# Performance work log

Hardware: AMD Instinct MI355X
Metric: run time of the kernel (lower is better)

Reference implementation:

```python
import jax, jax.numpy as jnp
import numpy as np

N_NODES = 50000
N_EDGES = 800000
N_GRAPHS = 64
IN_DIM = 128
HID = 128
S, C = 4, 16
DIM1 = 3 * S * S  # 48
OUT_DIM = DIM1 * C  # 768


def gcn_conv(x, W, b, src, dst, w):
    """PyG GCNConv: linear transform, then sym-normalized aggregation with self-loops (weight 1)."""
    n = x.shape[0]
    h = x @ W  # [N, out]
    deg = jnp.zeros((n,), x.dtype).at[dst].add(w) + 1.0  # self-loop weight 1
    dinv = jax.lax.rsqrt(deg)
    norm = dinv[src] * w * dinv[dst]  # [E]
    agg = jnp.zeros_like(h).at[dst].add(h[src] * norm[:, None])
    agg = agg + h * (1.0 / deg)[:, None]  # self-loop messages
    return agg + b


def setup_inputs() -> dict:
    key = jax.random.key(0)
    ks = jax.random.split(key, 16)
    x = jax.random.normal(ks[0], (N_NODES, IN_DIM), jnp.float32)
    edge_index = jax.random.randint(ks[1], (2, N_EDGES), 0, N_NODES, jnp.int64)
    edge_attr = jax.random.uniform(ks[2], (N_EDGES,), jnp.float32)
    batch = jnp.sort(jax.random.randint(ks[3], (N_NODES,), 0, N_GRAPHS, jnp.int64))

    def glorot(k, fan_in, fan_out):
        s = np.sqrt(6.0 / (fan_in + fan_out)).astype(np.float32)
        return jax.random.uniform(k, (fan_in, fan_out), jnp.float32, -s, s)

    return {
        "x": x, "edge_index": edge_index, "edge_attr": edge_attr, "batch": batch,
        "W1": glorot(ks[4], IN_DIM, HID), "b1": jnp.zeros((HID,), jnp.float32),
        "W2": glorot(ks[5], HID, HID // 2), "b2": jnp.zeros((HID // 2,), jnp.float32),
        "W3": glorot(ks[6], HID // 2, HID // 4), "b3": jnp.zeros((HID // 4,), jnp.float32),
        "Wl": glorot(ks[7], HID // 4, OUT_DIM), "bl": jnp.zeros((OUT_DIM,), jnp.float32),
    }


def reference(x, edge_index, edge_attr, batch, W1, b1, W2, b2, W3, b3, Wl, bl):
    src, dst = edge_index[0], edge_index[1]
    w = edge_attr / edge_attr.max()
    h = jax.nn.relu(gcn_conv(x, W1, b1, src, dst, w))
    h = jax.nn.relu(gcn_conv(h, W2, b2, src, dst, w))
    h = jax.nn.relu(gcn_conv(h, W3, b3, src, dst, w))
    # global mean pool over graphs
    sums = jax.ops.segment_sum(h, batch, num_segments=N_GRAPHS)
    cnt = jax.ops.segment_sum(jnp.ones((h.shape[0],), h.dtype), batch, num_segments=N_GRAPHS)
    pooled = sums / jnp.maximum(cnt, 1.0)[:, None]
    out = pooled @ Wl + bl  # [G, OUT_DIM]
    return out.reshape(N_GRAPHS, DIM1, C)
```

## Files before the change

### kernel.cpp

```cpp
#include <hip/hip_runtime.h>
#include <hip/hip_bf16.h>

#define NN 50000
#define NE 800000
#define NG 64
#define OUTD 768

#define G1B ((NN + 63) / 64)
#define SSEG 64
#define TTL 4
#define ESEG (NE / SSEG)
#define NTL (NN / TTL)
#define HRB (SSEG * TTL)
#define WB 16
#define MAXB 128
#define NB 196

#define W1E 2048
#define W2E 1024
#define W3E 256

__device__ __forceinline__ float bflo(unsigned int u) { return __uint_as_float(u << 16); }
__device__ __forceinline__ float bfhi(unsigned int u) { return __uint_as_float(u & 0xffff0000u); }
__device__ __forceinline__ unsigned short f2bf(float f) {
    unsigned int u = __float_as_uint(f);
    return (unsigned short)((u + 0x7fffu + ((u >> 16) & 1u)) >> 16);
}
__device__ __forceinline__ unsigned int pack2bf(float lo, float hi) {
    return (unsigned int)f2bf(lo) | ((unsigned int)f2bf(hi) << 16);
}

typedef __attribute__((ext_vector_type(8))) short bf16x8;
typedef __attribute__((ext_vector_type(4))) float f32x4;
union FragU { uint4 u4; bf16x8 v; };

__global__ __launch_bounds__(256) void prep_kernel(const float* __restrict__ W1,
                                                   const float* __restrict__ W2,
                                                   const float* __restrict__ W3,
                                                   uint4* __restrict__ f1,
                                                   uint4* __restrict__ f2,
                                                   uint4* __restrict__ f3,
                                                   const float* __restrict__ ea,
                                                   unsigned int* wmax) {
    const int b = blockIdx.x;
    if (b < WB) {
        for (int q = b * 256 + threadIdx.x; q < W1E + W2E + W3E; q += WB * 256) {
            const float* W; uint4* F; int N, qq;
            if (q < W1E) { W = W1; F = f1; N = 128; qq = q; }
            else if (q < W1E + W2E) { W = W2; F = f2; N = 64; qq = q - W1E; }
            else { W = W3; F = f3; N = 32; qq = q - W1E - W2E; }
            int lane = qq & 63, fi = qq >> 6;
            int NCT = N / 16, ct = fi % NCT, kc = fi / NCT;
            int col = ct * 16 + (lane & 15);
            int kb = kc * 32 + ((lane >> 4) << 3);
            uint4 w;
            w.x = pack2bf(W[(size_t)(kb + 0) * N + col], W[(size_t)(kb + 1) * N + col]);
            w.y = pack2bf(W[(size_t)(kb + 2) * N + col], W[(size_t)(kb + 3) * N + col]);
            w.z = pack2bf(W[(size_t)(kb + 4) * N + col], W[(size_t)(kb + 5) * N + col]);
            w.w = pack2bf(W[(size_t)(kb + 6) * N + col], W[(size_t)(kb + 7) * N + col]);
            F[qq] = w;
        }
    } else {
        __shared__ float red[256];
        const int bb = b - WB;
        float m = 0.0f;
        for (int i = bb * 256 + threadIdx.x; i < NE; i += MAXB * 256)
            m = fmaxf(m, ea[i]);
        red[threadIdx.x] = m;
        __syncthreads();
        for (int off = 128; off > 0; off >>= 1) {
            if (threadIdx.x < off)
                red[threadIdx.x] = fmaxf(red[threadIdx.x], red[threadIdx.x + off]);
            __syncthreads();
        }
        if (threadIdx.x == 0) atomicMax(wmax, __float_as_uint(red[0]));
    }
}

template <int K, int N, bool SCALE, typename TX>
__device__ __forceinline__ void mfma_gemm_tbl(const TX* __restrict__ X,
                                              const uint4* __restrict__ ftab,
                                              unsigned short* __restrict__ Y,
                                              const float* __restrict__ dinv,
                                              int nRows, int bx) {
    constexpr int NCT = N / 16;
    constexpr int KS = K / 32;
    const int tid = threadIdx.x;
    const int lane = tid & 63;
    const int wv = tid >> 6;
    const int m = lane & 15;
    const int quad = lane >> 4;
    const int row = bx * 64 + wv * 16 + m;
    const bool rowok = row < nRows;
    const TX* xr = X + (size_t)(rowok ? row : 0) * K;

    f32x4 acc[NCT];
#pragma unroll
    for (int ct = 0; ct < NCT; ++ct) acc[ct] = (f32x4){0.f, 0.f, 0.f, 0.f};

#pragma unroll
    for (int kc = 0; kc < KS; ++kc) {
        const int k0 = kc * 32 + quad * 8;
        FragU a;
        if constexpr (sizeof(TX) == 4) {
            float4 a0 = make_float4(0.f, 0.f, 0.f, 0.f), a1 = a0;
            if (rowok) {
                a0 = *(const float4*)(xr + k0);
                a1 = *(const float4*)(xr + k0 + 4);
            }
            a.u4 = make_uint4(pack2bf(a0.x, a0.y), pack2bf(a0.z, a0.w),
                              pack2bf(a1.x, a1.y), pack2bf(a1.z, a1.w));
        } else {
            a.u4 = rowok ? *(const uint4*)(xr + k0) : make_uint4(0, 0, 0, 0);
        }
#pragma unroll
        for (int ct = 0; ct < NCT; ++ct) {
            FragU b;
            b.u4 = ftab[(kc * NCT + ct) * 64 + lane];
            acc[ct] = __builtin_amdgcn_mfma_f32_16x16x32_bf16(a.v, b.v, acc[ct], 0, 0, 0);
        }
    }

    const int orowb = bx * 64 + wv * 16 + quad * 4;
    float dsc[4];
#pragma unroll
    for (int r = 0; r < 4; ++r)
        dsc[r] = SCALE ? ((orowb + r < nRows) ? dinv[orowb + r] : 1.0f) : 1.0f;
#pragma unroll
    for (int ct = 0; ct < NCT; ++ct) {
        int col = ct * 16 + m;
#pragma unroll
        for (int r = 0; r < 4; ++r) {
            int orow = orowb + r;
            if (orow < nRows) Y[(size_t)orow * N + col] = f2bf(dsc[r] * acc[ct][r]);
        }
    }
}

template <int K, int N, bool SCALE, typename TX>
__global__ __launch_bounds__(256) void mfma_gemm_kernel(const TX* __restrict__ X,
                                                        const uint4* __restrict__ ftab,
                                                        unsigned short* __restrict__ Y,
                                                        const float* __restrict__ dinv,
                                                        int nRows) {
    mfma_gemm_tbl<K, N, SCALE>(X, ftab, Y, dinv, nRows, blockIdx.x);
}

__global__ __launch_bounds__(256) void fused1_kernel(const float* __restrict__ x,
                                                     const uint4* __restrict__ f1,
                                                     unsigned short* __restrict__ bufA,
                                                     const int* __restrict__ dst,
                                                     int* __restrict__ rank,
                                                     unsigned short* __restrict__ pcnt) {
    extern __shared__ unsigned int lcnt[];
    const int b = blockIdx.x;
    if (b < G1B) {
        mfma_gemm_tbl<128, 128, false>(x, f1, bufA, nullptr, NN, b);
    } else {
        const int b2 = b - G1B;
        const int seg = b2 >> 2;
        const int tile = b2 & 3;
        for (int i = threadIdx.x; i < NTL / 2; i += 256) lcnt[i] = 0;
        __syncthreads();
        const int base = seg * ESEG;
        const int nlo = tile * NTL;
        for (int e = base + threadIdx.x; e < base + ESEG; e += 256) {
            int d = dst[e] - nlo;
            if ((unsigned)d < (unsigned)NTL) {
                unsigned int add = (d & 1) ? 0x10000u : 1u;
                unsigned int old = atomicAdd(&lcnt[d >> 1], add);
                rank[e] = (int)((old >> ((d & 1) * 16)) & 0xffffu);
            }
        }
        __syncthreads();
        unsigned int* prow32 = (unsigned int*)(pcnt + (size_t)seg * NN + nlo);
        for (int i = threadIdx.x; i < NTL / 2; i += 256) prow32[i] = lcnt[i];
    }
}

__device__ __forceinline__ void gridbar(unsigned int* bar, unsigned int target) {
    __syncthreads();
    if (threadIdx.x == 0) {
        __hip_atomic_fetch_add(bar, 1u, __ATOMIC_ACQ_REL, __HIP_MEMORY_SCOPE_AGENT);
        while (__hip_atomic_load(bar, __ATOMIC_ACQUIRE, __HIP_MEMORY_SCOPE_AGENT) < target)
            __builtin_amdgcn_s_sleep(2);
    }
    __syncthreads();
}

__global__ __launch_bounds__(256) void comb_scan_kernel(unsigned short* __restrict__ pcnt,
                                                        int* __restrict__ rowptr,
                                                        int* __restrict__ blocksum,
                                                        unsigned int* bar) {
    __shared__ int sh[256];
    const int tid = threadIdx.x;
    const int b = blockIdx.x;
    const int n = b * 256 + tid;

    int run = 0;
    if (n < NN) {
#pragma unroll
        for (int s = 0; s < SSEG; ++s) {
            size_t idx = (size_t)s * NN + n;
            int v = pcnt[idx];
            pcnt[idx] = (unsigned short)run;
            run += v;
        }
    }
    sh[tid] = run;
    __syncthreads();
    for (int off = 128; off > 0; off >>= 1) {
        if (tid < off) sh[tid] += sh[tid + off];
        __syncthreads();
    }
    if (tid == 0) blocksum[b] = sh[0];
    gridbar(bar, NB);

    int v2 = (tid < NB) ? blocksum[tid] : 0;
    __syncthreads();
    sh[tid] = v2;
    __syncthreads();
    for (int off = 1; off < 256; off <<= 1) {
        int t = (tid >= off) ? sh[tid - off] : 0;
        __syncthreads();
        sh[tid] += t;
        __syncthreads();
    }
    const int blockoff = (b > 0) ? sh[b - 1] : 0;
    if (b == 0 && tid == 0) rowptr[NN] = sh[NB - 1];
    __syncthreads();
    sh[tid] = run;
    __syncthreads();
    for (int off = 1; off < 256; off <<= 1) {
        int t = (tid >= off) ? sh[tid - off] : 0;
        __syncthreads();
        sh[tid] += t;
        __syncthreads();
    }
    if (n < NN) rowptr[n] = blockoff + sh[tid] - run;
}

__global__ void scat_kernel(const int* __restrict__ src, const int* __restrict__ dst,
                            const float* __restrict__ ea,
                            const int* __restrict__ rowptr,
                            const unsigned short* __restrict__ pcnt,
                            const int* __restrict__ rank,
                            const unsigned int* __restrict__ wmax,
                            int2* __restrict__ epack, int nE) {
    int e = blockIdx.x * blockDim.x + threadIdx.x;
    if (e >= nE) return;
    float rw = 1.0f / __uint_as_float(*wmax);
    int s = e / ESEG;
    int d = dst[e];
    int pos = rowptr[d] + (int)pcnt[(size_t)s * NN + d] + rank[e];
    epack[pos] = make_int2(src[e], __float_as_int(ea[e] * rw));
}

__global__ __launch_bounds__(256) void deg_scale_kernel(const int2* __restrict__ epack,
                                                        const int* __restrict__ rowptr,
                                                        float* __restrict__ dinv,
                                                        unsigned short* __restrict__ bufA) {
    __shared__ float sdinv[256];
    const int tid = threadIdx.x;
    const int b = blockIdx.x;
    const int n = b * 256 + tid;
    float di = 1.0f;
    if (n < NN) {
        int s0 = rowptr[n], s1 = rowptr[n + 1];
        float s = 1.0f;
        for (int e = s0; e < s1; ++e) s += __int_as_float(epack[e].y);
        di = rsqrtf(s);
        dinv[n] = di;
    }
    sdinv[tid] = di;
    __syncthreads();
    const int nrows = min(256, NN - b * 256);
    uint4* rows = (uint4*)bufA + (size_t)b * 256 * 16;
    for (int q = tid; q < nrows * 16; q += 256) {
        const float d = sdinv[q >> 4];
        uint4 u = rows[q];
        u.x = pack2bf(d * bflo(u.x), d * bfhi(u.x));
        u.y = pack2bf(d * bflo(u.y), d * bfhi(u.y));
        u.z = pack2bf(d * bflo(u.z), d * bfhi(u.z));
        u.w = pack2bf(d * bflo(u.w), d * bfhi(u.w));
        rows[q] = u;
    }
}

template <int D>
__global__ __launch_bounds__(256) void agg_kernel(const unsigned short* __restrict__ H,
                                                  const int* __restrict__ rowptr,
                                                  const int2* __restrict__ epack,
                                                  const float* __restrict__ dinv,
                                                  const float* __restrict__ bias,
                                                  unsigned short* __restrict__ out,
                                                  int nNodes) {
    constexpr int LPE = D / 8;
    constexpr int EPW = 64 / LPE;
    const int lane = threadIdx.x & 63;
    const int n = (blockIdx.x << 2) | (threadIdx.x >> 6);
    if (n >= nNodes) return;
    const int esub = lane / LPE;
    const int f8 = (lane % LPE) * 8;
    const int s0 = rowptr[n];
    const int cnt = rowptr[n + 1] - s0;

    float a[8] = {};
    int kb = 0;
    for (; kb + 2 * EPW <= cnt; kb += 2 * EPW) {
        const int2 pa = epack[s0 + kb + esub];
        const int2 pb = epack[s0 + kb + EPW + esub];
        const uint4 ua = *(const uint4*)(H + (size_t)pa.x * D + f8);
        const uint4 ub = *(const uint4*)(H + (size_t)pb.x * D + f8);
        const float ca = __int_as_float(pa.y);
        const float cb = __int_as_float(pb.y);
        a[0] = fmaf(ca, bflo(ua.x), a[0]); a[1] = fmaf(ca, bfhi(ua.x), a[1]);
        a[2] = fmaf(ca, bflo(ua.y), a[2]); a[3] = fmaf(ca, bfhi(ua.y), a[3]);
        a[4] = fmaf(ca, bflo(ua.z), a[4]); a[5] = fmaf(ca, bfhi(ua.z), a[5]);
        a[6] = fmaf(ca, bflo(ua.w), a[6]); a[7] = fmaf(ca, bfhi(ua.w), a[7]);
        a[0] = fmaf(cb, bflo(ub.x), a[0]); a[1] = fmaf(cb, bfhi(ub.x), a[1]);
        a[2] = fmaf(cb, bflo(ub.y), a[2]); a[3] = fmaf(cb, bfhi(ub.y), a[3]);
        a[4] = fmaf(cb, bflo(ub.z), a[4]); a[5] = fmaf(cb, bfhi(ub.z), a[5]);
        a[6] = fmaf(cb, bflo(ub.w), a[6]); a[7] = fmaf(cb, bfhi(ub.w), a[7]);
    }
    for (; kb < cnt; kb += EPW) {
        const int idx = kb + esub;
        const bool ok = idx < cnt;
        const int2 p = ok ? epack[s0 + idx] : make_int2(n, 0);
        const uint4 u = *(const uint4*)(H + (size_t)p.x * D + f8);
        const float c = ok ? __int_as_float(p.y) : 0.f;
        a[0] = fmaf(c, bflo(u.x), a[0]); a[1] = fmaf(c, bfhi(u.x), a[1]);
        a[2] = fmaf(c, bflo(u.y), a[2]); a[3] = fmaf(c, bfhi(u.y), a[3]);
        a[4] = fmaf(c, bflo(u.z), a[4]); a[5] = fmaf(c, bfhi(u.z), a[5]);
        a[6] = fmaf(c, bflo(u.w), a[6]); a[7] = fmaf(c, bfhi(u.w), a[7]);
    }
#pragma unroll
    for (int off = LPE; off < 64; off <<= 1) {
#pragma unroll
        for (int j = 0; j < 8; ++j) a[j] += __shfl_xor(a[j], off);
    }
    if (esub == 0) {
        const float di = dinv[n];
        const uint4 un = *(const uint4*)(H + (size_t)n * D + f8);
        const float4 b0 = *(const float4*)(bias + f8);
        const float4 b1 = *(const float4*)(bias + f8 + 4);
        float o[8];
        o[0] = fmaxf(fmaf(di, a[0] + bflo(un.x), b0.x), 0.f);
        o[1] = fmaxf(fmaf(di, a[1] + bfhi(un.x), b0.y), 0.f);
        o[2] = fmaxf(fmaf(di, a[2] + bflo(un.y), b0.z), 0.f);
        o[3] = fmaxf(fmaf(di, a[3] + bfhi(un.y), b0.w), 0.f);
        o[4] = fmaxf(fmaf(di, a[4] + bflo(un.z), b1.x), 0.f);
        o[5] = fmaxf(fmaf(di, a[5] + bfhi(un.z), b1.y), 0.f);
        o[6] = fmaxf(fmaf(di, a[6] + bflo(un.w), b1.z), 0.f);
        o[7] = fmaxf(fmaf(di, a[7] + bfhi(un.w), b1.w), 0.f);
        uint4 w;
        w.x = pack2bf(o[0], o[1]);
        w.y = pack2bf(o[2], o[3]);
        w.z = pack2bf(o[4], o[5]);
        w.w = pack2bf(o[6], o[7]);
        *(uint4*)(out + (size_t)n * D + f8) = w;
    }
}

__global__ __launch_bounds__(256) void pool2_kernel(const unsigned short* __restrict__ h,
                                                    const int* __restrict__ batch,
                                                    float* __restrict__ pooled, int n) {
    const int g = blockIdx.x;
    int lo = 0, hi = n;
    while (lo < hi) { int m = (lo + hi) >> 1; if (batch[m] < g) lo = m + 1; else hi = m; }
    const int start = lo;
    lo = start; hi = n;
    while (lo < hi) { int m = (lo + hi) >> 1; if (batch[m] < g + 1) lo = m + 1; else hi = m; }
    const int end = lo;

    __shared__ float part[256];
    const int f = threadIdx.x & 31;
    const int r = threadIdx.x >> 5;
    float acc = 0.f;
    for (int i = start + r; i < end; i += 8)
        acc += __uint_as_float((unsigned int)h[(size_t)i * 32 + f] << 16);
    part[threadIdx.x] = acc;
    __syncthreads();
    if (threadIdx.x < 32) {
        float s = 0.f;
#pragma unroll
        for (int q = 0; q < 8; ++q) s += part[q * 32 + f];
        float inv = 1.0f / fmaxf((float)(end - start), 1.0f);
        pooled[g * 32 + f] = s * inv;
    }
}

__global__ void final_kernel(const float* __restrict__ pooled,
                             const float* __restrict__ Wl, const float* __restrict__ bl,
                             float* __restrict__ out) {
    int idx = blockIdx.x * blockDim.x + threadIdx.x;
    int g = idx / OUTD, o = idx - g * OUTD;
    float acc = bl[o];
#pragma unroll
    for (int k = 0; k < 32; ++k)
        acc = fmaf(pooled[g * 32 + k], Wl[k * OUTD + o], acc);
    out[idx] = acc;
}

extern "C" void kernel_launch(void* const* d_in, const int* in_sizes, int n_in,
                              void* d_out, int out_size, void* d_ws, size_t ws_size,
                              hipStream_t stream) {
    const float* x = (const float*)d_in[0];
    const int* eidx = (const int*)d_in[1];
    const float* ea = (const float*)d_in[2];
    const int* batch = (const int*)d_in[3];
    const float* W1 = (const float*)d_in[4];
    const float* b1 = (const float*)d_in[5];
    const float* W2 = (const float*)d_in[6];
    const float* b2 = (const float*)d_in[7];
    const float* W3 = (const float*)d_in[8];
    const float* b3 = (const float*)d_in[9];
    const float* Wl = (const float*)d_in[10];
    const float* bl = (const float*)d_in[11];
    const int* src = eidx;
    const int* dst = eidx + NE;

    char* p = (char*)d_ws;
    auto take = [&](size_t bytes) {
        char* r = p;
        p += (bytes + 255) & ~(size_t)255;
        return r;
    };
    float* dinv = (float*)take(NN * 4);
    int* rowptr = (int*)take((NN + 1) * 4);
    int* blocksum = (int*)take(256 * 4);
    int2* epack = (int2*)take((size_t)NE * 8);
    float* pooled = (float*)take(NG * 32 * 4);
    unsigned int* wmaxbar = (unsigned int*)take(8);
    uint4* f1 = (uint4*)take(W1E * 16);
    uint4* f2 = (uint4*)take(W2E * 16);
    uint4* f3 = (uint4*)take(W3E * 16);
    unsigned short* bufA = (unsigned short*)take((size_t)NN * 128 * 2);
    unsigned short* bufB = (unsigned short*)take((size_t)NN * 128 * 2);
    int* rank = (int*)bufB;
    unsigned short* pcnt = (unsigned short*)((char*)bufB + (size_t)NE * 4 + 256);

    unsigned int* wmax = wmaxbar;
    unsigned int* bar = wmaxbar + 1;

    const int nblk = (NN + 255) / 256;
    const int eblk = (NE + 255) / 256;

    hipMemsetAsync(wmaxbar, 0, 8, stream);

    prep_kernel<<<WB + MAXB, 256, 0, stream>>>(W1, W2, W3, f1, f2, f3, ea, wmax);
    fused1_kernel<<<G1B + HRB, 256, (NTL / 2) * 4, stream>>>(x, f1, bufA, dst, rank, pcnt);
    comb_scan_kernel<<<NB, 256, 0, stream>>>(pcnt, rowptr, blocksum, bar);
    scat_kernel<<<eblk, 256, 0, stream>>>(src, dst, ea, rowptr, pcnt, rank, wmax, epack, NE);
    deg_scale_kernel<<<nblk, 256, 0, stream>>>(epack, rowptr, dinv, bufA);

    agg_kernel<128><<<(NN + 3) / 4, 256, 0, stream>>>(bufA, rowptr, epack, dinv, b1, bufB, NN);
    mfma_gemm_kernel<128, 64, true, unsigned short>
        <<<G1B, 256, 0, stream>>>(bufB, f2, bufA, dinv, NN);
    agg_kernel<64><<<(NN + 3) / 4, 256, 0, stream>>>(bufA, rowptr, epack, dinv, b2, bufB, NN);
    mfma_gemm_kernel<64, 32, true, unsigned short>
        <<<G1B, 256, 0, stream>>>(bufB, f3, bufA, dinv, NN);
    agg_kernel<32><<<(NN + 3) / 4, 256, 0, stream>>>(bufA, rowptr, epack, dinv, b3, bufB, NN);

    pool2_kernel<<<NG, 256, 0, stream>>>(bufB, batch, pooled, NN);
    final_kernel<<<(NG * OUTD) / 256, 256, 0, stream>>>(pooled, Wl, bl, (float*)d_out);
}
```

Baseline: 301.1 us.

## Split aggregation into feature slices, fold source dinv into agg, fuse pool+final

The aggregation kernels now assign each block a 32-feature slice, with 4 lanes per edge and 16 edges per wave, instead of covering the full feature width per node. Block indices are interleaved so slices of neighbouring nodes run close together in time. The first layer drops the separate pass that rescaled H1 in place by dinv and instead multiplies each edge coefficient by dinv[src] inside the aggregation, leaving only a small degree kernel. Pooling and the final linear layer are merged into one kernel. The slicing aims to shrink the working set per gather and raise parallelism, but it re-reads the edge lists once per slice and adds a dinv gather per edge in layer 1.

```diff
diff --git a/kernel.cpp b/kernel.cpp
--- a/kernel.cpp
+++ b/kernel.cpp
@@ -256,38 +256,17 @@
     epack[pos] = make_int2(src[e], __float_as_int(ea[e] * rw));
 }
 
-__global__ __launch_bounds__(256) void deg_scale_kernel(const int2* __restrict__ epack,
-                                                        const int* __restrict__ rowptr,
-                                                        float* __restrict__ dinv,
-                                                        unsigned short* __restrict__ bufA) {
-    __shared__ float sdinv[256];
-    const int tid = threadIdx.x;
-    const int b = blockIdx.x;
-    const int n = b * 256 + tid;
-    float di = 1.0f;
-    if (n < NN) {
-        int s0 = rowptr[n], s1 = rowptr[n + 1];
-        float s = 1.0f;
-        for (int e = s0; e < s1; ++e) s += __int_as_float(epack[e].y);
-        di = rsqrtf(s);
-        dinv[n] = di;
-    }
-    sdinv[tid] = di;
-    __syncthreads();
-    const int nrows = min(256, NN - b * 256);
-    uint4* rows = (uint4*)bufA + (size_t)b * 256 * 16;
-    for (int q = tid; q < nrows * 16; q += 256) {
-        const float d = sdinv[q >> 4];
-        uint4 u = rows[q];
-        u.x = pack2bf(d * bflo(u.x), d * bfhi(u.x));
-        u.y = pack2bf(d * bflo(u.y), d * bfhi(u.y));
-        u.z = pack2bf(d * bflo(u.z), d * bfhi(u.z));
-        u.w = pack2bf(d * bflo(u.w), d * bfhi(u.w));
-        rows[q] = u;
-    }
-}
-
-template <int D>
+__global__ void deg_kernel(const int2* __restrict__ epack, const int* __restrict__ rowptr,
+                           float* __restrict__ dinv, int n) {
+    int i = blockIdx.x * blockDim.x + threadIdx.x;
+    if (i >= n) return;
+    int s0 = rowptr[i], s1 = rowptr[i + 1];
+    float s = 1.0f;
+    for (int e = s0; e < s1; ++e) s += __int_as_float(epack[e].y);
+    dinv[i] = rsqrtf(s);
+}
+
+template <int D, bool DSRC>
 __global__ __launch_bounds__(256) void agg_kernel(const unsigned short* __restrict__ H,
                                                   const int* __restrict__ rowptr,
                                                   const int2* __restrict__ epack,
@@ -295,13 +274,19 @@
                                                   const float* __restrict__ bias,
                                                   unsigned short* __restrict__ out,
                                                   int nNodes) {
-    constexpr int LPE = D / 8;
-    constexpr int EPW = 64 / LPE;
+    constexpr int NQ = D / 32;
+    constexpr int LPE = 4;
+    constexpr int EPW = 16;
+    const int b = blockIdx.x;
+    int slice, idx;
+    if constexpr (NQ == 4) { slice = (b & 7) >> 1; idx = (b >> 3) * 2 + (b & 1); }
+    else if constexpr (NQ == 2) { slice = (b & 7) >> 2; idx = (b >> 3) * 4 + (b & 3); }
+    else { slice = 0; idx = b; }
     const int lane = threadIdx.x & 63;
-    const int n = (blockIdx.x << 2) | (threadIdx.x >> 6);
+    const int n = idx * 4 + (threadIdx.x >> 6);
     if (n >= nNodes) return;
-    const int esub = lane / LPE;
-    const int f8 = (lane % LPE) * 8;
+    const int esub = lane >> 2;
+    const int f8 = slice * 32 + (lane & 3) * 8;
     const int s0 = rowptr[n];
     const int cnt = rowptr[n + 1] - s0;
 
@@ -312,8 +297,9 @@
         const int2 pb = epack[s0 + kb + EPW + esub];
         const uint4 ua = *(const uint4*)(H + (size_t)pa.x * D + f8);
         const uint4 ub = *(const uint4*)(H + (size_t)pb.x * D + f8);
-        const float ca = __int_as_float(pa.y);
-        const float cb = __int_as_float(pb.y);
+        float ca = __int_as_float(pa.y);
+        float cb = __int_as_float(pb.y);
+        if constexpr (DSRC) { ca *= dinv[pa.x]; cb *= dinv[pb.x]; }
         a[0] = fmaf(ca, bflo(ua.x), a[0]); a[1] = fmaf(ca, bfhi(ua.x), a[1]);
         a[2] = fmaf(ca, bflo(ua.y), a[2]); a[3] = fmaf(ca, bfhi(ua.y), a[3]);
         a[4] = fmaf(ca, bflo(ua.z), a[4]); a[5] = fmaf(ca, bfhi(ua.z), a[5]);
@@ -324,11 +310,12 @@
         a[6] = fmaf(cb, bflo(ub.w), a[6]); a[7] = fmaf(cb, bfhi(ub.w), a[7]);
     }
     for (; kb < cnt; kb += EPW) {
-        const int idx = kb + esub;
-        const bool ok = idx < cnt;
-        const int2 p = ok ? epack[s0 + idx] : make_int2(n, 0);
+        const int idx2 = kb + esub;
+        const bool ok = idx2 < cnt;
+        const int2 p = ok ? epack[s0 + idx2] : make_int2(n, 0);
         const uint4 u = *(const uint4*)(H + (size_t)p.x * D + f8);
-        const float c = ok ? __int_as_float(p.y) : 0.f;
+        float c = ok ? __int_as_float(p.y) : 0.f;
+        if constexpr (DSRC) c *= dinv[p.x];
         a[0] = fmaf(c, bflo(u.x), a[0]); a[1] = fmaf(c, bfhi(u.x), a[1]);
         a[2] = fmaf(c, bflo(u.y), a[2]); a[3] = fmaf(c, bfhi(u.y), a[3]);
         a[4] = fmaf(c, bflo(u.z), a[4]); a[5] = fmaf(c, bfhi(u.z), a[5]);
@@ -341,18 +328,19 @@
     }
     if (esub == 0) {
         const float di = dinv[n];
+        const float ss = DSRC ? di : 1.0f;
         const uint4 un = *(const uint4*)(H + (size_t)n * D + f8);
         const float4 b0 = *(const float4*)(bias + f8);
         const float4 b1 = *(const float4*)(bias + f8 + 4);
         float o[8];
-        o[0] = fmaxf(fmaf(di, a[0] + bflo(un.x), b0.x), 0.f);
-        o[1] = fmaxf(fmaf(di, a[1] + bfhi(un.x), b0.y), 0.f);
-        o[2] = fmaxf(fmaf(di, a[2] + bflo(un.y), b0.z), 0.f);
-        o[3] = fmaxf(fmaf(di, a[3] + bfhi(un.y), b0.w), 0.f);
-        o[4] = fmaxf(fmaf(di, a[4] + bflo(un.z), b1.x), 0.f);
-        o[5] = fmaxf(fmaf(di, a[5] + bfhi(un.z), b1.y), 0.f);
-        o[6] = fmaxf(fmaf(di, a[6] + bflo(un.w), b1.z), 0.f);
-        o[7] = fmaxf(fmaf(di, a[7] + bfhi(un.w), b1.w), 0.f);
+        o[0] = fmaxf(fmaf(di, fmaf(ss, bflo(un.x), a[0]), b0.x), 0.f);
+        o[1] = fmaxf(fmaf(di, fmaf(ss, bfhi(un.x), a[1]), b0.y), 0.f);
+        o[2] = fmaxf(fmaf(di, fmaf(ss, bflo(un.y), a[2]), b0.z), 0.f);
+        o[3] = fmaxf(fmaf(di, fmaf(ss, bfhi(un.y), a[3]), b0.w), 0.f);
+        o[4] = fmaxf(fmaf(di, fmaf(ss, bflo(un.z), a[4]), b1.x), 0.f);
+        o[5] = fmaxf(fmaf(di, fmaf(ss, bfhi(un.z), a[5]), b1.y), 0.f);
+        o[6] = fmaxf(fmaf(di, fmaf(ss, bflo(un.w), a[6]), b1.z), 0.f);
+        o[7] = fmaxf(fmaf(di, fmaf(ss, bfhi(un.w), a[7]), b1.w), 0.f);
         uint4 w;
         w.x = pack2bf(o[0], o[1]);
         w.y = pack2bf(o[2], o[3]);
@@ -362,9 +350,11 @@
     }
 }
 
-__global__ __launch_bounds__(256) void pool2_kernel(const unsigned short* __restrict__ h,
-                                                    const int* __restrict__ batch,
-                                                    float* __restrict__ pooled, int n) {
+__global__ __launch_bounds__(256) void poolfinal_kernel(const unsigned short* __restrict__ h,
+                                                        const int* __restrict__ batch,
+                                                        const float* __restrict__ Wl,
+                                                        const float* __restrict__ bl,
+                                                        float* __restrict__ out, int n) {
     const int g = blockIdx.x;
     int lo = 0, hi = n;
     while (lo < hi) { int m = (lo + hi) >> 1; if (batch[m] < g) lo = m + 1; else hi = m; }
@@ -374,6 +364,7 @@
     const int end = lo;
 
     __shared__ float part[256];
+    __shared__ float pooled[32];
     const int f = threadIdx.x & 31;
     const int r = threadIdx.x >> 5;
     float acc = 0.f;
@@ -386,20 +377,15 @@
 #pragma unroll
         for (int q = 0; q < 8; ++q) s += part[q * 32 + f];
         float inv = 1.0f / fmaxf((float)(end - start), 1.0f);
-        pooled[g * 32 + f] = s * inv;
-    }
-}
-
-__global__ void final_kernel(const float* __restrict__ pooled,
-                             const float* __restrict__ Wl, const float* __restrict__ bl,
-                             float* __restrict__ out) {
-    int idx = blockIdx.x * blockDim.x + threadIdx.x;
-    int g = idx / OUTD, o = idx - g * OUTD;
-    float acc = bl[o];
-#pragma unroll
-    for (int k = 0; k < 32; ++k)
-        acc = fmaf(pooled[g * 32 + k], Wl[k * OUTD + o], acc);
-    out[idx] = acc;
+        pooled[f] = s * inv;
+    }
+    __syncthreads();
+    for (int o = threadIdx.x; o < OUTD; o += 256) {
+        float a = bl[o];
+#pragma unroll
+        for (int k = 0; k < 32; ++k) a = fmaf(pooled[k], Wl[k * OUTD + o], a);
+        out[(size_t)g * OUTD + o] = a;
+    }
 }
 
 extern "C" void kernel_launch(void* const* d_in, const int* in_sizes, int n_in,
@@ -430,7 +416,6 @@
     int* rowptr = (int*)take((NN + 1) * 4);
     int* blocksum = (int*)take(256 * 4);
     int2* epack = (int2*)take((size_t)NE * 8);
-    float* pooled = (float*)take(NG * 32 * 4);
     unsigned int* wmaxbar = (unsigned int*)take(8);
     uint4* f1 = (uint4*)take(W1E * 16);
     uint4* f2 = (uint4*)take(W2E * 16);
@@ -452,16 +437,15 @@
     fused1_kernel<<<G1B + HRB, 256, (NTL / 2) * 4, stream>>>(x, f1, bufA, dst, rank, pcnt);
     comb_scan_kernel<<<NB, 256, 0, stream>>>(pcnt, rowptr, blocksum, bar);
     scat_kernel<<<eblk, 256, 0, stream>>>(src, dst, ea, rowptr, pcnt, rank, wmax, epack, NE);
-    deg_scale_kernel<<<nblk, 256, 0, stream>>>(epack, rowptr, dinv, bufA);
-
-    agg_kernel<128><<<(NN + 3) / 4, 256, 0, stream>>>(bufA, rowptr, epack, dinv, b1, bufB, NN);
+    deg_kernel<<<nblk, 256, 0, stream>>>(epack, rowptr, dinv, NN);
+
+    agg_kernel<128, true><<<NN, 256, 0, stream>>>(bufA, rowptr, epack, dinv, b1, bufB, NN);
     mfma_gemm_kernel<128, 64, true, unsigned short>
         <<<G1B, 256, 0, stream>>>(bufB, f2, bufA, dinv, NN);
-    agg_kernel<64><<<(NN + 3) / 4, 256, 0, stream>>>(bufA, rowptr, epack, dinv, b2, bufB, NN);
+    agg_kernel<64, false><<<NN / 2, 256, 0, stream>>>(bufA, rowptr, epack, dinv, b2, bufB, NN);
     mfma_gemm_kernel<64, 32, true, unsigned short>
         <<<G1B, 256, 0, stream>>>(bufB, f3, bufA, dinv, NN);
-    agg_kernel<32><<<(NN + 3) / 4, 256, 0, stream>>>(bufA, rowptr, epack, dinv, b3, bufB, NN);
-
-    pool2_kernel<<<NG, 256, 0, stream>>>(bufB, batch, pooled, NN);
-    final_kernel<<<(NG * OUTD) / 256, 256, 0, stream>>>(pooled, Wl, bl, (float*)d_out);
-}
+    agg_kernel<32, false><<<NN / 4, 256, 0, stream>>>(bufA, rowptr, epack, dinv, b3, bufB, NN);
+
+    poolfinal_kernel<<<NG, 256, 0, stream>>>(bufB, batch, Wl, bl, (float*)d_out, NN);
+}
```

New measurement: 360.4 us. 19.7% more time.
